# Optimization experiments

Hardware: AMD Instinct MI355X
Metric: run time of the kernel (lower is better)

The kernel has to match this reference:

```python
import jax, jax.numpy as jnp
import numpy as np
from jax import lax

B, T = 2048, 256
V, E, H = 128, 128, 64
POS_WEIGHT = 20.0


def setup_inputs() -> dict:
    key = jax.random.key(0)
    ks = jax.random.split(key, 9)
    # indices in [1, V) so padding_idx=0 row (zeroed) is unused
    x = jax.random.randint(ks[0], (B, T), 1, V)
    targets = (jax.random.uniform(ks[1], (B,)) < 0.05).astype(jnp.float32)
    emb = jax.random.normal(ks[2], (V, E), dtype=jnp.float32).at[0].set(0.0)  # padding_idx=0
    k = 1.0 / np.sqrt(H)
    W_ih = jax.random.uniform(ks[3], (4 * H, E), minval=-k, maxval=k, dtype=jnp.float32)
    W_hh = jax.random.uniform(ks[4], (4 * H, H), minval=-k, maxval=k, dtype=jnp.float32)
    b_ih = jax.random.uniform(ks[5], (4 * H,), minval=-k, maxval=k, dtype=jnp.float32)
    b_hh = jax.random.uniform(ks[6], (4 * H,), minval=-k, maxval=k, dtype=jnp.float32)
    W_fc = jax.random.uniform(ks[7], (1, H), minval=-k, maxval=k, dtype=jnp.float32)
    b_fc = jax.random.uniform(ks[8], (1,), minval=-k, maxval=k, dtype=jnp.float32)
    return {"x": x, "targets": targets, "emb": emb, "W_ih": W_ih, "W_hh": W_hh,
            "b_ih": b_ih, "b_hh": b_hh, "W_fc": W_fc, "b_fc": b_fc}


def reference(x, targets, emb, W_ih, W_hh, b_ih, b_hh, W_fc, b_fc):
    xe = emb[x]  # [B, T, E]
    # precompute input-to-hidden projections for all timesteps: [B, T, 4H]
    xp = jnp.einsum('bte,ge->btg', xe, W_ih) + b_ih + b_hh
    h0 = jnp.zeros((xe.shape[0], W_hh.shape[1]), dtype=xe.dtype)
    c0 = jnp.zeros_like(h0)

    def step(carry, xt):
        h, c = carry
        gates = xt + h @ W_hh.T  # [B, 4H], PyTorch gate order: i, f, g, o
        i, f, g, o = jnp.split(gates, 4, axis=-1)
        c = jax.nn.sigmoid(f) * c + jax.nn.sigmoid(i) * jnp.tanh(g)
        h = jax.nn.sigmoid(o) * jnp.tanh(c)
        return (h, c), None

    (hT, _), _ = lax.scan(step, (h0, c0), jnp.swapaxes(xp, 0, 1))  # scan over time
    logits = (hT @ W_fc.T + b_fc)[:, 0]  # [B]
    # BCEWithLogits with pos_weight, mean reduction (numerically stable)
    loss = -(POS_WEIGHT * targets * jax.nn.log_sigmoid(logits)
             + (1.0 - targets) * jax.nn.log_sigmoid(-logits)).mean()
    return logits, loss
```

## Files before the change

kernel.cpp:

```cpp
#include <hip/hip_runtime.h>
#include <stdint.h>

#define B_ 2048
#define T_ 256
#define V_ 128
#define E_ 128
#define H_ 64
#define G4_ 256
#define POS_W 20.0f
#define MB_ 4
#define NBLK_ (B_ / MB_)
typedef _Float16 half1;
typedef __attribute__((ext_vector_type(8))) _Float16 f16x8;
typedef __attribute__((ext_vector_type(4))) float f32x4;

#if __has_builtin(__builtin_amdgcn_exp2f)
#define EXP2F(x) __builtin_amdgcn_exp2f(x)
#else
#define EXP2F(x) exp2f(x)
#endif

#if __has_builtin(__builtin_amdgcn_rcpf)
#define RCPF(x) __builtin_amdgcn_rcpf(x)
#else
#define RCPF(x) (1.0f / (x))
#endif

__device__ __forceinline__ float sigm(float x) {
    return RCPF(1.0f + EXP2F(-1.44269504f * x));
}
__device__ __forceinline__ float tanhr(float x) {
    float t = EXP2F(2.88539008f * x);
    return 1.0f - 2.0f * RCPF(t + 1.0f);
}

__device__ __forceinline__ void lds_barrier() {
    asm volatile("s_waitcnt lgkmcnt(0)\n\ts_barrier" ::: "memory");
}

__global__ void k_prep(const float* __restrict__ emb, const float* __restrict__ Wih,
                       const float* __restrict__ bih, const float* __restrict__ bhh,
                       float* __restrict__ projC, float* __restrict__ loss_slot) {
    int tid = threadIdx.x;
    int v = blockIdx.x;
    if (v == 0 && tid == 0) *loss_slot = 0.0f;
    int u = tid >> 2, g = tid & 3;
    int row = g * 64 + u;
    const float4* e4 = (const float4*)(emb + v * E_);
    const float4* w4 = (const float4*)(Wih + row * E_);
    float acc = bih[row] + bhh[row];
#pragma unroll
    for (int i = 0; i < E_ / 4; ++i) {
        float4 a = e4[i];
        float4 b = w4[i];
        acc += a.x * b.x + a.y * b.y + a.z * b.z + a.w * b.w;
    }
    projC[v * G4_ + tid] = acc;
}

__launch_bounds__(256, 2)
__global__ void k_lstm(const int* __restrict__ x, const float* __restrict__ Whh,
                       const float* __restrict__ projC, const float* __restrict__ Wfc,
                       const float* __restrict__ bfc, const float* __restrict__ targets,
                       float* __restrict__ logits, float* __restrict__ loss_slot) {
    int b0 = blockIdx.x * MB_;
    int t = threadIdx.x;
    int w = t >> 6, l = t & 63;
    int q = l >> 4, cc = l & 15;
    int u = 16 * w + cc;

    __shared__ __align__(16) half1 hf[2][1024];
    __shared__ int xT[T_][MB_];
    __shared__ float hfin[MB_][68];
    __shared__ float zred[MB_];

#pragma unroll
    for (int i = 0; i < MB_; ++i) xT[t][i] = x[(b0 + i) * T_ + t];
    ((float*)hf)[t] = 0.0f;
    ((float*)hf)[t + 256] = 0.0f;
    ((float*)hf)[t + 512] = 0.0f;
    ((float*)hf)[t + 768] = 0.0f;
    __syncthreads();

    f16x8 bf[4][2];
#pragma unroll
    for (int jj = 0; jj < 4; ++jj) {
#pragma unroll
        for (int c = 0; c < 2; ++c) {
            int row = jj * 64 + 16 * w + cc;
            int kb = c * 32 + q * 8;
            float4 w0 = *(const float4*)(Whh + row * H_ + kb);
            float4 w1 = *(const float4*)(Whh + row * H_ + kb + 4);
            f16x8 tmp;
            tmp[0] = (half1)w0.x; tmp[1] = (half1)w0.y;
            tmp[2] = (half1)w0.z; tmp[3] = (half1)w0.w;
            tmp[4] = (half1)w1.x; tmp[5] = (half1)w1.y;
            tmp[6] = (half1)w1.z; tmp[7] = (half1)w1.w;
            bf[jj][c] = tmp;
        }
    }

    int hbase = (u >> 5) * 512 + ((u >> 3) & 3) * 128 + (4 * q) * 8 + (u & 7);

    float cA = 0.0f, hA = 0.0f;

    f32x4 ppA = *(const f32x4*)(projC + xT[0][q] * G4_ + u * 4);
    f32x4 pnA = *(const f32x4*)(projC + xT[1][q] * G4_ + u * 4);

    if (blockIdx.x & 1) {
        asm volatile("s_sleep 7");
    }

    int p = 0;
#pragma unroll 2
    for (int step = 0; step < T_; ++step) {
        f32x4 p2A = *(const f32x4*)(projC + xT[(step + 2) & (T_ - 1)][q] * G4_ + u * 4);

        const f16x8 a0 = *(const f16x8*)(hf[p] + l * 8);
        const f16x8 a1 = *(const f16x8*)(hf[p] + 512 + l * 8);

        f32x4 z4 = {0.0f, 0.0f, 0.0f, 0.0f};
        float gA[4];
#pragma unroll
        for (int jj = 0; jj < 4; ++jj) {
            f32x4 d0 = __builtin_amdgcn_mfma_f32_16x16x32_f16(a0, bf[jj][0], z4, 0, 0, 0);
            f32x4 d1 = __builtin_amdgcn_mfma_f32_16x16x32_f16(a1, bf[jj][1], z4, 0, 0, 0);
            gA[jj] = d0[0] + d1[0];
        }

        float iA = sigm(gA[0] + ppA.x);
        float fA = sigm(gA[1] + ppA.y);
        float ggA = tanhr(gA[2] + ppA.z);
        float oA = sigm(gA[3] + ppA.w);
        cA = fA * cA + iA * ggA;
        hA = oA * tanhr(cA);

        hf[p ^ 1][hbase] = (half1)hA;

        ppA = pnA;
        pnA = p2A;
        p ^= 1;
        lds_barrier();
    }

    hfin[q][u] = hA;
    __syncthreads();
    int m4 = t >> 6, uu = t & 63;
    float part = hfin[m4][uu] * Wfc[uu];
#pragma unroll
    for (int off = 32; off > 0; off >>= 1) part += __shfl_down(part, off, 64);
    if (uu == 0) {
        float z = part + bfc[0];
        logits[b0 + m4] = z;
        float tg = targets[b0 + m4];
        float e = EXP2F(-1.44269504f * fabsf(z));
        float lsp = fminf(z, 0.0f) - log1pf(e);
        float lsn = lsp - z;
        zred[m4] = -(POS_W * tg * lsp + (1.0f - tg) * lsn) * (1.0f / (float)B_);
    }
    __syncthreads();
    if (t == 0) {
        float s = 0.0f;
#pragma unroll
        for (int i = 0; i < MB_; ++i) s += zred[i];
        atomicAdd(loss_slot, s);
    }
}

extern "C" void kernel_launch(void* const* d_in, const int* in_sizes, int n_in,
                              void* d_out, int out_size, void* d_ws, size_t ws_size,
                              hipStream_t stream) {
    const int* x = (const int*)d_in[0];
    const float* targets = (const float*)d_in[1];
    const float* emb = (const float*)d_in[2];
    const float* Wih = (const float*)d_in[3];
    const float* Whh = (const float*)d_in[4];
    const float* bih = (const float*)d_in[5];
    const float* bhh = (const float*)d_in[6];
    const float* Wfc = (const float*)d_in[7];
    const float* bfc = (const float*)d_in[8];
    float* out = (float*)d_out;

    float* projC = (float*)d_ws;

    k_prep<<<dim3(V_), dim3(256), 0, stream>>>(emb, Wih, bih, bhh, projC, out + B_);
    k_lstm<<<dim3(NBLK_), dim3(256), 0, stream>>>(x, Whh, projC, Wfc, bfc, targets, out,
                                                  out + B_);
}
```

Before: 164.9 us.

## Process eight sequences per block using spare MFMA output rows

Each block now handles 8 batch rows instead of 4. The second group of four reuses the otherwise unused rows of the 16x16 MFMA output, with its hidden state stored at an offset in the shared h buffer. The two K-half MFMAs are now chained through the accumulator instead of being added afterwards. This halves the grid, so there is one block per CU (launch bounds lowered), and the s_sleep staggering between blocks is dropped. The aim is to get more useful work out of each MFMA and each barrier per recurrence step. In exchange, each thread does twice the gate math on a serial chain, and there is no longer a second block per CU to hide latency.

New measurement: 170.3 us. 1.03x slower.

```diff
diff --git a/kernel.cpp b/kernel.cpp
--- a/kernel.cpp
+++ b/kernel.cpp
@@ -8,7 +8,7 @@
 #define H_ 64
 #define G4_ 256
 #define POS_W 20.0f
-#define MB_ 4
+#define MB_ 8
 #define NBLK_ (B_ / MB_)
 typedef _Float16 half1;
 typedef __attribute__((ext_vector_type(8))) _Float16 f16x8;
@@ -58,7 +58,7 @@
     projC[v * G4_ + tid] = acc;
 }
 
-__launch_bounds__(256, 2)
+__launch_bounds__(256, 1)
 __global__ void k_lstm(const int* __restrict__ x, const float* __restrict__ Whh,
                        const float* __restrict__ projC, const float* __restrict__ Wfc,
                        const float* __restrict__ bfc, const float* __restrict__ targets,
@@ -103,29 +103,31 @@
     int hbase = (u >> 5) * 512 + ((u >> 3) & 3) * 128 + (4 * q) * 8 + (u & 7);
 
     float cA = 0.0f, hA = 0.0f;
+    float cB = 0.0f, hB = 0.0f;
 
     f32x4 ppA = *(const f32x4*)(projC + xT[0][q] * G4_ + u * 4);
+    f32x4 ppB = *(const f32x4*)(projC + xT[0][q + 4] * G4_ + u * 4);
     f32x4 pnA = *(const f32x4*)(projC + xT[1][q] * G4_ + u * 4);
-
-    if (blockIdx.x & 1) {
-        asm volatile("s_sleep 7");
-    }
+    f32x4 pnB = *(const f32x4*)(projC + xT[1][q + 4] * G4_ + u * 4);
 
     int p = 0;
 #pragma unroll 2
     for (int step = 0; step < T_; ++step) {
-        f32x4 p2A = *(const f32x4*)(projC + xT[(step + 2) & (T_ - 1)][q] * G4_ + u * 4);
+        int t2 = (step + 2) & (T_ - 1);
+        f32x4 p2A = *(const f32x4*)(projC + xT[t2][q] * G4_ + u * 4);
+        f32x4 p2B = *(const f32x4*)(projC + xT[t2][q + 4] * G4_ + u * 4);
 
         const f16x8 a0 = *(const f16x8*)(hf[p] + l * 8);
         const f16x8 a1 = *(const f16x8*)(hf[p] + 512 + l * 8);
 
         f32x4 z4 = {0.0f, 0.0f, 0.0f, 0.0f};
-        float gA[4];
+        float gA[4], gB[4];
 #pragma unroll
         for (int jj = 0; jj < 4; ++jj) {
             f32x4 d0 = __builtin_amdgcn_mfma_f32_16x16x32_f16(a0, bf[jj][0], z4, 0, 0, 0);
-            f32x4 d1 = __builtin_amdgcn_mfma_f32_16x16x32_f16(a1, bf[jj][1], z4, 0, 0, 0);
-            gA[jj] = d0[0] + d1[0];
+            f32x4 d = __builtin_amdgcn_mfma_f32_16x16x32_f16(a1, bf[jj][1], d0, 0, 0, 0);
+            gA[jj] = d[0];
+            gB[jj] = d[1];
         }
 
         float iA = sigm(gA[0] + ppA.x);
@@ -135,28 +137,50 @@
         cA = fA * cA + iA * ggA;
         hA = oA * tanhr(cA);
 
+        float iB = sigm(gB[0] + ppB.x);
+        float fB = sigm(gB[1] + ppB.y);
+        float ggB = tanhr(gB[2] + ppB.z);
+        float oB = sigm(gB[3] + ppB.w);
+        cB = fB * cB + iB * ggB;
+        hB = oB * tanhr(cB);
+
         hf[p ^ 1][hbase] = (half1)hA;
-
-        ppA = pnA;
-        pnA = p2A;
+        hf[p ^ 1][hbase + 8] = (half1)hB;
+
+        ppA = pnA; ppB = pnB;
+        pnA = p2A; pnB = p2B;
         p ^= 1;
         lds_barrier();
     }
 
     hfin[q][u] = hA;
+    hfin[q + 4][u] = hB;
     __syncthreads();
     int m4 = t >> 6, uu = t & 63;
-    float part = hfin[m4][uu] * Wfc[uu];
-#pragma unroll
-    for (int off = 32; off > 0; off >>= 1) part += __shfl_down(part, off, 64);
+    float wv = Wfc[uu];
+    float pa = hfin[m4][uu] * wv;
+    float pb = hfin[m4 + 4][uu] * wv;
+#pragma unroll
+    for (int off = 32; off > 0; off >>= 1) {
+        pa += __shfl_down(pa, off, 64);
+        pb += __shfl_down(pb, off, 64);
+    }
     if (uu == 0) {
-        float z = part + bfc[0];
+        float z = pa + bfc[0];
         logits[b0 + m4] = z;
         float tg = targets[b0 + m4];
         float e = EXP2F(-1.44269504f * fabsf(z));
         float lsp = fminf(z, 0.0f) - log1pf(e);
         float lsn = lsp - z;
         zred[m4] = -(POS_W * tg * lsp + (1.0f - tg) * lsn) * (1.0f / (float)B_);
+
+        float z2 = pb + bfc[0];
+        logits[b0 + m4 + 4] = z2;
+        float tg2 = targets[b0 + m4 + 4];
+        float e2 = EXP2F(-1.44269504f * fabsf(z2));
+        float lsp2 = fminf(z2, 0.0f) - log1pf(e2);
+        float lsn2 = lsp2 - z2;
+        zred[m4 + 4] = -(POS_W * tg2 * lsp2 + (1.0f - tg2) * lsn2) * (1.0f / (float)B_);
     }
     __syncthreads();
     if (t == 0) {
```

## Run each LSTM batch tile in one wavefront with register-level hidden-state exchange

Applied to the files above, without the earlier changes.

Collapses the 4-wave block into a single 64-lane wavefront that computes all 64 hidden units for its 4 sequences, keeping 32 f16 weight fragments in registers. The hidden state is redistributed between steps with ds_bpermute and byte permutes instead of an LDS write plus block barrier, which removes the per-step s_barrier. Token indices are pre-shifted to byte offsets, and gate preactivations are fused into FMAs before exp2. In exchange each wave does four times the MFMA and transcendental work serially, and register pressure rises, which may limit latency hiding.

Result: slower. 288.6 us (+75.0%).

```diff
diff --git a/kernel.cpp b/kernel.cpp
--- a/kernel.cpp
+++ b/kernel.cpp
@@ -13,6 +13,7 @@
 typedef _Float16 half1;
 typedef __attribute__((ext_vector_type(8))) _Float16 f16x8;
 typedef __attribute__((ext_vector_type(4))) float f32x4;
+typedef __attribute__((ext_vector_type(4))) int i32x4;
 
 #if __has_builtin(__builtin_amdgcn_exp2f)
 #define EXP2F(x) __builtin_amdgcn_exp2f(x)
@@ -26,16 +27,15 @@
 #define RCPF(x) (1.0f / (x))
 #endif
 
-__device__ __forceinline__ float sigm(float x) {
-    return RCPF(1.0f + EXP2F(-1.44269504f * x));
-}
 __device__ __forceinline__ float tanhr(float x) {
     float t = EXP2F(2.88539008f * x);
     return 1.0f - 2.0f * RCPF(t + 1.0f);
 }
 
-__device__ __forceinline__ void lds_barrier() {
-    asm volatile("s_waitcnt lgkmcnt(0)\n\ts_barrier" ::: "memory");
+__device__ __forceinline__ unsigned f16bits(half1 h) {
+    union { half1 h; unsigned short u; } v;
+    v.h = h;
+    return (unsigned)v.u;
 }
 
 __global__ void k_prep(const float* __restrict__ emb, const float* __restrict__ Wih,
@@ -58,113 +58,132 @@
     projC[v * G4_ + tid] = acc;
 }
 
-__launch_bounds__(256, 2)
+__launch_bounds__(64, 1)
 __global__ void k_lstm(const int* __restrict__ x, const float* __restrict__ Whh,
                        const float* __restrict__ projC, const float* __restrict__ Wfc,
                        const float* __restrict__ bfc, const float* __restrict__ targets,
                        float* __restrict__ logits, float* __restrict__ loss_slot) {
     int b0 = blockIdx.x * MB_;
-    int t = threadIdx.x;
-    int w = t >> 6, l = t & 63;
-    int q = l >> 4, cc = l & 15;
-    int u = 16 * w + cc;
-
-    __shared__ __align__(16) half1 hf[2][1024];
+    int l = threadIdx.x;
+    int hi = l >> 4, cc = l & 15;
+
     __shared__ int xT[T_][MB_];
-    __shared__ float hfin[MB_][68];
-    __shared__ float zred[MB_];
-
-#pragma unroll
-    for (int i = 0; i < MB_; ++i) xT[t][i] = x[(b0 + i) * T_ + t];
-    ((float*)hf)[t] = 0.0f;
-    ((float*)hf)[t + 256] = 0.0f;
-    ((float*)hf)[t + 512] = 0.0f;
-    ((float*)hf)[t + 768] = 0.0f;
-    __syncthreads();
-
-    f16x8 bf[4][2];
-#pragma unroll
-    for (int jj = 0; jj < 4; ++jj) {
-#pragma unroll
-        for (int c = 0; c < 2; ++c) {
-            int row = jj * 64 + 16 * w + cc;
-            int kb = c * 32 + q * 8;
-            float4 w0 = *(const float4*)(Whh + row * H_ + kb);
-            float4 w1 = *(const float4*)(Whh + row * H_ + kb + 4);
-            f16x8 tmp;
-            tmp[0] = (half1)w0.x; tmp[1] = (half1)w0.y;
-            tmp[2] = (half1)w0.z; tmp[3] = (half1)w0.w;
-            tmp[4] = (half1)w1.x; tmp[5] = (half1)w1.y;
-            tmp[6] = (half1)w1.z; tmp[7] = (half1)w1.w;
-            bf[jj][c] = tmp;
-        }
-    }
-
-    int hbase = (u >> 5) * 512 + ((u >> 3) & 3) * 128 + (4 * q) * 8 + (u & 7);
-
-    float cA = 0.0f, hA = 0.0f;
-
-    f32x4 ppA = *(const f32x4*)(projC + xT[0][q] * G4_ + u * 4);
-    f32x4 pnA = *(const f32x4*)(projC + xT[1][q] * G4_ + u * 4);
-
-    if (blockIdx.x & 1) {
-        asm volatile("s_sleep 7");
-    }
-
-    int p = 0;
-#pragma unroll 2
-    for (int step = 0; step < T_; ++step) {
-        f32x4 p2A = *(const f32x4*)(projC + xT[(step + 2) & (T_ - 1)][q] * G4_ + u * 4);
-
-        const f16x8 a0 = *(const f16x8*)(hf[p] + l * 8);
-        const f16x8 a1 = *(const f16x8*)(hf[p] + 512 + l * 8);
-
-        f32x4 z4 = {0.0f, 0.0f, 0.0f, 0.0f};
-        float gA[4];
-#pragma unroll
-        for (int jj = 0; jj < 4; ++jj) {
-            f32x4 d0 = __builtin_amdgcn_mfma_f32_16x16x32_f16(a0, bf[jj][0], z4, 0, 0, 0);
-            f32x4 d1 = __builtin_amdgcn_mfma_f32_16x16x32_f16(a1, bf[jj][1], z4, 0, 0, 0);
-            gA[jj] = d0[0] + d1[0];
-        }
-
-        float iA = sigm(gA[0] + ppA.x);
-        float fA = sigm(gA[1] + ppA.y);
-        float ggA = tanhr(gA[2] + ppA.z);
-        float oA = sigm(gA[3] + ppA.w);
-        cA = fA * cA + iA * ggA;
-        hA = oA * tanhr(cA);
-
-        hf[p ^ 1][hbase] = (half1)hA;
-
-        ppA = pnA;
-        pnA = p2A;
-        p ^= 1;
-        lds_barrier();
-    }
-
-    hfin[q][u] = hA;
-    __syncthreads();
-    int m4 = t >> 6, uu = t & 63;
-    float part = hfin[m4][uu] * Wfc[uu];
-#pragma unroll
-    for (int off = 32; off > 0; off >>= 1) part += __shfl_down(part, off, 64);
-    if (uu == 0) {
-        float z = part + bfc[0];
-        logits[b0 + m4] = z;
-        float tg = targets[b0 + m4];
-        float e = EXP2F(-1.44269504f * fabsf(z));
-        float lsp = fminf(z, 0.0f) - log1pf(e);
-        float lsn = lsp - z;
-        zred[m4] = -(POS_W * tg * lsp + (1.0f - tg) * lsn) * (1.0f / (float)B_);
+    for (int i = l; i < T_ * MB_; i += 64) {
+        int tt = i >> 2, rr = i & 3;
+        xT[tt][rr] = x[(b0 + rr) * T_ + tt] << 10;
     }
     __syncthreads();
-    if (t == 0) {
-        float s = 0.0f;
-#pragma unroll
-        for (int i = 0; i < MB_; ++i) s += zred[i];
-        atomicAdd(loss_slot, s);
+
+    f16x8 bf[4][4][2];
+#pragma unroll
+    for (int g = 0; g < 4; ++g)
+#pragma unroll
+        for (int n = 0; n < 4; ++n)
+#pragma unroll
+            for (int c = 0; c < 2; ++c) {
+                int row = g * 64 + 16 * n + cc;
+                int kb = c * 32 + hi * 8;
+                float4 w0 = *(const float4*)(Whh + row * H_ + kb);
+                float4 w1 = *(const float4*)(Whh + row * H_ + kb + 4);
+                f16x8 tmp;
+                tmp[0] = (half1)w0.x; tmp[1] = (half1)w0.y;
+                tmp[2] = (half1)w0.z; tmp[3] = (half1)w0.w;
+                tmp[4] = (half1)w1.x; tmp[5] = (half1)w1.y;
+                tmp[6] = (half1)w1.z; tmp[7] = (half1)w1.w;
+                bf[g][n][c] = tmp;
+            }
+
+    int abase = ((cc >> 2) << 6) + ((hi & 1) << 5);
+    unsigned sel = (hi & 2) ? 0x07060302u : 0x05040100u;
+
+    const char* pcb = (const char*)projC + cc * 16;
+    float ccell[4] = {0.f, 0.f, 0.f, 0.f};
+    float hkeep[4] = {0.f, 0.f, 0.f, 0.f};
+    f16x8 a0, a1;
+#pragma unroll
+    for (int j = 0; j < 8; ++j) { a0[j] = (half1)0.f; a1[j] = (half1)0.f; }
+
+    f32x4 pp[4], pn[4];
+    int tok0 = xT[0][hi];
+#pragma unroll
+    for (int n = 0; n < 4; ++n) pp[n] = *(const f32x4*)(pcb + tok0 + n * 256);
+    int xc = xT[1][hi];
+
+    const f32x4 z4 = {0.f, 0.f, 0.f, 0.f};
+#pragma unroll 1
+    for (int step = 0; step < T_; ++step) {
+#pragma unroll
+        for (int n = 0; n < 4; ++n) pn[n] = *(const f32x4*)(pcb + xc + n * 256);
+        int xn = xT[(step + 2) & (T_ - 1)][hi];
+
+        float G[4][4];
+#pragma unroll
+        for (int n = 0; n < 4; ++n)
+#pragma unroll
+            for (int g = 0; g < 4; ++g) {
+                f32x4 d0 = __builtin_amdgcn_mfma_f32_16x16x32_f16(a0, bf[g][n][0], z4, 0, 0, 0);
+                f32x4 d = __builtin_amdgcn_mfma_f32_16x16x32_f16(a1, bf[g][n][1], d0, 0, 0, 0);
+                G[n][g] = d[0];
+            }
+
+        unsigned us[4];
+#pragma unroll
+        for (int n = 0; n < 4; ++n) {
+            float psx = -1.44269504f * pp[n][0];
+            float psy = -1.44269504f * pp[n][1];
+            float pgz = 2.88539008f * pp[n][2];
+            float psw = -1.44269504f * pp[n][3];
+            float i_ = RCPF(1.0f + EXP2F(__builtin_fmaf(-1.44269504f, G[n][0], psx)));
+            float f_ = RCPF(1.0f + EXP2F(__builtin_fmaf(-1.44269504f, G[n][1], psy)));
+            float tg = 1.0f - 2.0f * RCPF(EXP2F(__builtin_fmaf(2.88539008f, G[n][2], pgz)) + 1.0f);
+            float o_ = RCPF(1.0f + EXP2F(__builtin_fmaf(-1.44269504f, G[n][3], psw)));
+            float cn = __builtin_fmaf(f_, ccell[n], i_ * tg);
+            ccell[n] = cn;
+            float hn = o_ * tanhr(cn);
+            hkeep[n] = hn;
+            us[n] = f16bits((half1)hn);
+        }
+        unsigned hp01 = us[0] | (us[1] << 16);
+        unsigned hp23 = us[2] | (us[3] << 16);
+
+        int r01[8], r23[8];
+#pragma unroll
+        for (int j = 0; j < 8; ++j) {
+            int ad = abase + 4 * j;
+            r01[j] = __builtin_amdgcn_ds_bpermute(ad, (int)hp01);
+            r23[j] = __builtin_amdgcn_ds_bpermute(ad, (int)hp23);
+        }
+        i32x4 A0, A1;
+#pragma unroll
+        for (int k = 0; k < 4; ++k) {
+            A0[k] = (int)__builtin_amdgcn_perm((unsigned)r01[2 * k + 1], (unsigned)r01[2 * k], sel);
+            A1[k] = (int)__builtin_amdgcn_perm((unsigned)r23[2 * k + 1], (unsigned)r23[2 * k], sel);
+        }
+        a0 = __builtin_bit_cast(f16x8, A0);
+        a1 = __builtin_bit_cast(f16x8, A1);
+
+#pragma unroll
+        for (int n = 0; n < 4; ++n) pp[n] = pn[n];
+        xc = xn;
     }
+
+    float part = 0.f;
+#pragma unroll
+    for (int n = 0; n < 4; ++n) part += hkeep[n] * Wfc[16 * n + cc];
+#pragma unroll
+    for (int off = 8; off > 0; off >>= 1) part += __shfl_down(part, off, 16);
+    float rsum = __shfl(part, l & 48, 64);
+    float z = rsum + bfc[0];
+    if (cc == 0) logits[b0 + hi] = z;
+    float tg = targets[b0 + hi];
+    float e = EXP2F(-1.44269504f * fabsf(z));
+    float lsp = fminf(z, 0.0f) - log1pf(e);
+    float lsn = lsp - z;
+    float lp = -(POS_W * tg * lsp + (1.0f - tg) * lsn) * (1.0f / (float)B_);
+    float s = 0.f;
+#pragma unroll
+    for (int qq = 0; qq < 4; ++qq) s += __shfl(lp, qq * 16, 64);
+    if (l == 0) atomicAdd(loss_slot, s);
 }
 
 extern "C" void kernel_launch(void* const* d_in, const int* in_sizes, int n_in,
@@ -184,6 +203,6 @@
     float* projC = (float*)d_ws;
 
     k_prep<<<dim3(V_), dim3(256), 0, stream>>>(emb, Wih, bih, bhh, projC, out + B_);
-    k_lstm<<<dim3(NBLK_), dim3(256), 0, stream>>>(x, Whh, projC, Wfc, bfc, targets, out,
-                                                  out + B_);
-}
+    k_lstm<<<dim3(NBLK_), dim3(64), 0, stream>>>(x, Whh, projC, Wfc, bfc, targets, out,
+                                                 out + B_);
+}
```
